# Optimization experiments

Hardware: AMD Instinct MI355X
Metric: run time of the kernel (lower is better)

Reference implementation:

```python
import jax, jax.numpy as jnp
import numpy as np

N = 100000   # total nodes across the batch
D = 3        # ambient dimension of the point cloud
T = 64       # num_thetas (directions)
R = 64       # resolution of the ECT discretization
B = 128      # number of point clouds in the batch
RADIUS = 1.1
SCALE = 8.0


def setup_inputs() -> dict:
    key = jax.random.key(0)
    kx, kv, kb = jax.random.split(key, 3)
    x = jax.random.normal(kx, (N, D), dtype=jnp.float32)
    # directions; the layer stores v movedim'd and moves it back, so math uses [D, T]
    v = jax.random.normal(kv, (D, T), dtype=jnp.float32)
    v = v / jnp.linalg.norm(v, axis=0, keepdims=True)  # unit directions, typical usage
    batch = jnp.sort(jax.random.randint(kb, (N,), 0, B, dtype=jnp.int64))
    return {"x": x, "v": v, "batch": batch}


def reference(x, v, batch):
    # compute_ect_points:
    # nh[n,t] = <x_n, v_t>
    nh = x @ v  # [N, T]
    lin = jnp.linspace(-RADIUS, RADIUS, R, dtype=x.dtype)  # [R]
    # ecc[n,t,r] = sigmoid(scale * (lin[r] - nh[n,t]))  -- large [N,T,R] intermediate
    ecc = jax.nn.sigmoid(SCALE * (lin[None, None, :] - nh[:, :, None]))
    # scatter-sum over the batch index (index_add): -> [B, T, R]
    ect = jax.ops.segment_sum(ecc, batch, num_segments=B)
    # normalized=False -> return ect.squeeze(); no singleton dims here
    return ect
```

## Files before the change

kernel.cpp:

```cpp
#include <hip/hip_runtime.h>
#include <math.h>


#define THREADS 256
#define TPB 4
#define TQ  16
#define PAD 63
#define STEPS 148
#define ROW32 228
#define ROW64 114
#define HO_BASE64 (TPB * ROW64)

constexpr double cexp_taylor(double r) {
    double s = 1.0, term = 1.0;
    for (int i = 1; i < 18; ++i) { term *= r / (double)i; s += term; }
    return s;
}
constexpr double cexp(double x) {
    const double LN2 = 0.69314718055994530942;
    const int n = (int)(x / LN2 + (x >= 0.0 ? 0.5 : -0.5));
    const double r = x - (double)n * LN2;
    double e = cexp_taylor(r);
    if (n >= 0) { for (int i = 0; i < n;  ++i) e *= 2.0; }
    else        { for (int i = 0; i < -n; ++i) e *= 0.5; }
    return e;
}
struct WTab {
    float w[STEPS];
    constexpr WTab() : w() {
        const double d = 2.2 / 63.0;
        for (int j = 0; j < STEPS; ++j) {
            const double z = 8.0 * d * (double)(111 - j);
            w[j] = (float)(1.0 / ((1.0 + cexp(-z)) * 65536.0));
        }
    }
};
constexpr WTab WT;

__device__ __forceinline__ int lb64(const int* __restrict__ A, int n, int val,
                                    int lane) {
    int lo = 0, hi = n;
    while (hi - lo > 64) {
        const long long span = hi - lo;
        const int p = lo + (int)((span * lane) >> 6);
        const unsigned long long m = __ballot(A[p] < val);
        const int c = __popcll(m);
        if (c == 0) { hi = lo; break; }
        const int plast = lo + (int)((span * (c - 1)) >> 6);
        const int pnext = (c < 64) ? (lo + (int)((span * (long long)c) >> 6)) : hi;
        lo = plast + 1; hi = pnext;
    }
    const int span = hi - lo;
    const unsigned long long m = __ballot(lane < span && A[lo + lane] < val);
    return lo + __popcll(m);
}

__global__ __launch_bounds__(THREADS, 8) void ect_fused6_kernel(
    const float* __restrict__ x,
    const float* __restrict__ v,
    const int*   __restrict__ batch,
    float* __restrict__ out,
    int n, float inv_d, float bias)
{
    __shared__ unsigned long long Hu[2 * TPB * ROW64];

    const int tid  = threadIdx.x;
    const int wv   = tid >> 6;
    const int lane = tid & 63;
    const int b    = blockIdx.x >> 4;
    const int tq   = blockIdx.x & (TQ - 1);

    for (int i = tid; i < 2 * TPB * ROW64; i += THREADS) Hu[i] = 0ull;

    const int s0 = lb64(batch, n, b, lane);
    const int s1 = lb64(batch, n, b + 1, lane);

    const int t_l  = lane >> 4;
    const int slot = (lane & 15) + (wv << 4);
    const int tbase = tq * TPB;
    const int t    = tbase + t_l;
    const float va = v[t], vb = v[64 + t], vc = v[128 + t];
    const int rowoff64 = t_l * ROW64;

    __syncthreads();

    for (int base = s0; base < s1; base += 4 * 64) {
        float xs0[4], xs1[4], xs2[4];
        bool  ok[4];
#pragma unroll
        for (int k = 0; k < 4; ++k) {
            const int idx = base + (k << 6) + slot;
            ok[k] = (idx < s1);
            if (ok[k]) {
                const float3 xx = *(const float3*)(x + 3 * (size_t)idx);
                xs0[k] = xx.x; xs1[k] = xx.y; xs2[k] = xx.z;
            }
        }
#pragma unroll
        for (int k = 0; k < 4; ++k) {
            if (!ok[k]) continue;
            const float nh = fmaf(xs0[k], va, fmaf(xs1[k], vb, xs2[k] * vc));
            float bin = fmaf(nh, inv_d, bias);
            bin = fminf(fmaxf(bin, 0.0f), 158.999f);
            const float g0f = floorf(bin);
            const float fr  = bin - g0f;
            const int   a   = PAD + (int)g0f;
            const unsigned q1 = (unsigned)(fr * 65536.0f + 0.5f);
            const unsigned q0 = 65536u - q1;
            const unsigned long long val =
                (unsigned long long)q0 | ((unsigned long long)q1 << 32);
            const int w64 = (a >> 1) + rowoff64 + ((a & 1) ? HO_BASE64 : 0);
            atomicAdd(&Hu[w64], val);
        }
    }

    __syncthreads();

    {
        unsigned* He32 = (unsigned*)Hu;
        unsigned* Ho32 = (unsigned*)(Hu + HO_BASE64);
        if (tid < ROW32) {
#pragma unroll
            for (int tt = 0; tt < TPB; ++tt) {
                const int i = tt * ROW32 + tid;
                unsigned s = He32[i];
                if (tid > 0) s += Ho32[i - 1];
                ((float*)He32)[i] = (float)s;
            }
        }
    }

    __syncthreads();

    const float* H = (const float*)Hu + wv * ROW32 + lane;
    float a0 = 0.f, a1 = 0.f;
#pragma unroll
    for (int j = 0; j < STEPS; j += 2) {
        a0 = fmaf(WT.w[j],     H[j],     a0);
        a1 = fmaf(WT.w[j + 1], H[j + 1], a1);
    }
    out[((size_t)b * 64 + tbase + wv) * 64 + lane] = a0 + a1;
}

extern "C" void kernel_launch(void* const* d_in, const int* in_sizes, int n_in,
                              void* d_out, int out_size, void* d_ws, size_t ws_size,
                              hipStream_t stream) {
    const float* x     = (const float*)d_in[0];
    const float* v     = (const float*)d_in[1];
    const int*   batch = (const int*)d_in[2];
    float*       out   = (float*)d_out;

    const int n = in_sizes[0] / 3;

    const double d = 2.2 / 63.0;
    const float inv_d = (float)(1.0 / d);
    const float bias  = 79.5f;

    hipLaunchKernelGGL(ect_fused6_kernel, dim3(128 * TQ), dim3(THREADS), 0,
                       stream, x, v, batch, out, n, inv_d, bias);
}
```

Measured before the change: 17.52 us.

## Precompute segment bounds in a separate kernel and shorten weighted sum with suffix sums

A new pre-pass kernel writes per-batch segment start offsets into workspace, which replaces the per-block wave-parallel binary search over the batch array. In the main kernel, the first 60 sigmoid weights are treated as saturated to one. Their contribution is computed as a difference of wave-level suffix sums of the histogram, which leaves fewer FMA steps per output. The cost is a second kernel launch and extra shared memory plus shuffle work. Rows are also widened to 256, which changes the LDS footprint and may reduce occupancy. Treating those weights as exactly one introduces a small approximation error.

New measurement: 20.30 us. 1.16x slower.

```diff
diff --git a/kernel.cpp b/kernel.cpp
--- a/kernel.cpp
+++ b/kernel.cpp
@@ -7,9 +7,11 @@
 #define TQ  16
 #define PAD 63
 #define STEPS 148
-#define ROW32 228
-#define ROW64 114
+#define J0 60
+#define ROW32 256
+#define ROW64 128
 #define HO_BASE64 (TPB * ROW64)
+#define BSEG 128
 
 constexpr double cexp_taylor(double r) {
     double s = 1.0, term = 1.0;
@@ -37,32 +39,40 @@
 };
 constexpr WTab WT;
 
-__device__ __forceinline__ int lb64(const int* __restrict__ A, int n, int val,
-                                    int lane) {
-    int lo = 0, hi = n;
-    while (hi - lo > 64) {
-        const long long span = hi - lo;
-        const int p = lo + (int)((span * lane) >> 6);
-        const unsigned long long m = __ballot(A[p] < val);
-        const int c = __popcll(m);
-        if (c == 0) { hi = lo; break; }
-        const int plast = lo + (int)((span * (c - 1)) >> 6);
-        const int pnext = (c < 64) ? (lo + (int)((span * (long long)c) >> 6)) : hi;
-        lo = plast + 1; hi = pnext;
+__device__ __forceinline__ float wave_suffix(float x, int lane) {
+#pragma unroll
+    for (int d = 1; d < 64; d <<= 1) {
+        const float y = __shfl_down(x, d, 64);
+        x += (lane + d < 64) ? y : 0.0f;
     }
-    const int span = hi - lo;
-    const unsigned long long m = __ballot(lane < span && A[lo + lane] < val);
-    return lo + __popcll(m);
+    return x;
 }
 
-__global__ __launch_bounds__(THREADS, 8) void ect_fused6_kernel(
+__global__ void seg_bounds_kernel(const int* __restrict__ batch,
+                                  int* __restrict__ seg, int n) {
+    int i = blockIdx.x * blockDim.x + threadIdx.x;
+    if (i >= n) return;
+    const int a = batch[i];
+    if (i == 0) {
+        for (int bb = 0; bb <= a; ++bb) seg[bb] = 0;
+    } else {
+        const int p = batch[i - 1];
+        for (int bb = p + 1; bb <= a; ++bb) seg[bb] = i;
+    }
+    if (i == n - 1) {
+        for (int bb = a + 1; bb <= BSEG; ++bb) seg[bb] = n;
+    }
+}
+
+__global__ __launch_bounds__(THREADS, 8) void ect_fused8_kernel(
     const float* __restrict__ x,
     const float* __restrict__ v,
-    const int*   __restrict__ batch,
+    const int*   __restrict__ seg,
     float* __restrict__ out,
-    int n, float inv_d, float bias)
+    float inv_d, float bias)
 {
     __shared__ unsigned long long Hu[2 * TPB * ROW64];
+    __shared__ float Slds[TPB][128];
 
     const int tid  = threadIdx.x;
     const int wv   = tid >> 6;
@@ -72,8 +82,7 @@
 
     for (int i = tid; i < 2 * TPB * ROW64; i += THREADS) Hu[i] = 0ull;
 
-    const int s0 = lb64(batch, n, b, lane);
-    const int s1 = lb64(batch, n, b + 1, lane);
+    const int s0 = seg[b], s1 = seg[b + 1];
 
     const int t_l  = lane >> 4;
     const int slot = (lane & 15) + (wv << 4);
@@ -119,23 +128,37 @@
     {
         unsigned* He32 = (unsigned*)Hu;
         unsigned* Ho32 = (unsigned*)(Hu + HO_BASE64);
-        if (tid < ROW32) {
-#pragma unroll
-            for (int tt = 0; tt < TPB; ++tt) {
-                const int i = tt * ROW32 + tid;
-                unsigned s = He32[i];
-                if (tid > 0) s += Ho32[i - 1];
-                ((float*)He32)[i] = (float)s;
-            }
+        for (int i = tid; i < TPB * ROW32; i += THREADS) {
+            const int a = i & (ROW32 - 1);
+            unsigned s = He32[i];
+            if (a > 0) s += Ho32[i - 1];
+            ((float*)He32)[i] = (float)s;
         }
     }
 
     __syncthreads();
 
+    {
+        const float* HF = (const float*)Hu + wv * ROW32;
+        const float c0 = HF[lane],       c1 = HF[64 + lane];
+        const float c2 = HF[128 + lane], c3 = HF[192 + lane];
+        float tot23 = c2 + c3;
+#pragma unroll
+        for (int d = 1; d < 64; d <<= 1) tot23 += __shfl_xor(tot23, d, 64);
+        const float s1v = wave_suffix(c1, lane) + tot23;
+        const float carry = __shfl(s1v, 0, 64);
+        const float s0v = wave_suffix(c0, lane) + carry;
+        Slds[wv][lane]      = s0v;
+        Slds[wv][64 + lane] = s1v;
+    }
+
+    __syncthreads();
+
     const float* H = (const float*)Hu + wv * ROW32 + lane;
-    float a0 = 0.f, a1 = 0.f;
+    float a0 = (Slds[wv][lane] - Slds[wv][lane + J0]) * (1.0f / 65536.0f);
+    float a1 = 0.f;
 #pragma unroll
-    for (int j = 0; j < STEPS; j += 2) {
+    for (int j = J0; j < STEPS; j += 2) {
         a0 = fmaf(WT.w[j],     H[j],     a0);
         a1 = fmaf(WT.w[j + 1], H[j + 1], a1);
     }
@@ -152,10 +175,14 @@
 
     const int n = in_sizes[0] / 3;
 
+    int* seg = (int*)d_ws;
+
     const double d = 2.2 / 63.0;
     const float inv_d = (float)(1.0 / d);
     const float bias  = 79.5f;
 
-    hipLaunchKernelGGL(ect_fused6_kernel, dim3(128 * TQ), dim3(THREADS), 0,
-                       stream, x, v, batch, out, n, inv_d, bias);
+    hipLaunchKernelGGL(seg_bounds_kernel, dim3((n + THREADS - 1) / THREADS),
+                       dim3(THREADS), 0, stream, batch, seg, n);
+    hipLaunchKernelGGL(ect_fused8_kernel, dim3(BSEG * TQ), dim3(THREADS), 0,
+                       stream, x, v, seg, out, inv_d, bias);
 }
```

## Replace saturated sigmoid taps with suffix-sum window and use guessed scalar segment search

Applied to the files above, without the earlier changes.

The per-output convolution over 148 sigmoid weights is shortened to 80 taps. The far bins where the weight is essentially 1 are folded into a single suffix sum computed with wave shuffles, and the histogram rows are padded to 256 so each wave converts its own row. The wave-wide ballot lower-bound search is replaced by a scalar binary search that starts from a window guessed from a uniform batch distribution and falls back to a full search if the guess is wrong. This saves FMA and LDS reads in the epilogue but adds shuffle reductions and treats weights beyond the window as exactly 1, which is a slight approximation.

New measurement: 17.80 us. About the same (+1.6%).

```diff
diff --git a/kernel.cpp b/kernel.cpp
--- a/kernel.cpp
+++ b/kernel.cpp
@@ -6,10 +6,12 @@
 #define TPB 4
 #define TQ  16
 #define PAD 63
-#define STEPS 148
-#define ROW32 228
-#define ROW64 114
+#define J0  64
+#define STEPS 144
+#define ROW32 256
+#define ROW64 128
 #define HO_BASE64 (TPB * ROW64)
+#define BSEG 128
 
 constexpr double cexp_taylor(double r) {
     double s = 1.0, term = 1.0;
@@ -37,25 +39,32 @@
 };
 constexpr WTab WT;
 
-__device__ __forceinline__ int lb64(const int* __restrict__ A, int n, int val,
-                                    int lane) {
-    int lo = 0, hi = n;
-    while (hi - lo > 64) {
-        const long long span = hi - lo;
-        const int p = lo + (int)((span * lane) >> 6);
-        const unsigned long long m = __ballot(A[p] < val);
-        const int c = __popcll(m);
-        if (c == 0) { hi = lo; break; }
-        const int plast = lo + (int)((span * (c - 1)) >> 6);
-        const int pnext = (c < 64) ? (lo + (int)((span * (long long)c) >> 6)) : hi;
-        lo = plast + 1; hi = pnext;
+__device__ __forceinline__ float wave_suffix(float x, int lane) {
+#pragma unroll
+    for (int d = 1; d < 64; d <<= 1) {
+        const float y = __shfl_down(x, d, 64);
+        x += (lane + d < 64) ? y : 0.0f;
     }
-    const int span = hi - lo;
-    const unsigned long long m = __ballot(lane < span && A[lo + lane] < val);
-    return lo + __popcll(m);
+    return x;
 }
 
-__global__ __launch_bounds__(THREADS, 8) void ect_fused6_kernel(
+__device__ __forceinline__ int lower_scalar(const int* __restrict__ A, int n,
+                                            int val) {
+    const long long g = ((long long)val * (long long)n) >> 7;
+    int lo = (int)(g - 1024 > 0 ? g - 1024 : 0);
+    int hi = (int)(g + 1024 < n ? g + 1024 : n);
+    const bool okl = (lo == 0) || (A[__builtin_amdgcn_readfirstlane(lo - 1)] < val);
+    const bool okh = (hi == n) || (A[__builtin_amdgcn_readfirstlane(hi)] >= val);
+    if (!(okl && okh)) { lo = 0; hi = n; }
+    while (hi > lo) {
+        const int mid = (lo + hi) >> 1;
+        const int key = A[__builtin_amdgcn_readfirstlane(mid)];
+        if (key < val) lo = mid + 1; else hi = mid;
+    }
+    return lo;
+}
+
+__global__ __launch_bounds__(THREADS, 8) void ect_fused9_kernel(
     const float* __restrict__ x,
     const float* __restrict__ v,
     const int*   __restrict__ batch,
@@ -72,8 +81,8 @@
 
     for (int i = tid; i < 2 * TPB * ROW64; i += THREADS) Hu[i] = 0ull;
 
-    const int s0 = lb64(batch, n, b, lane);
-    const int s1 = lb64(batch, n, b + 1, lane);
+    const int s0 = lower_scalar(batch, n, b);
+    const int s1 = lower_scalar(batch, n, b + 1);
 
     const int t_l  = lane >> 4;
     const int slot = (lane & 15) + (wv << 4);
@@ -116,26 +125,36 @@
 
     __syncthreads();
 
+    float c[4];
     {
-        unsigned* He32 = (unsigned*)Hu;
-        unsigned* Ho32 = (unsigned*)(Hu + HO_BASE64);
-        if (tid < ROW32) {
+        const unsigned* He32 = (const unsigned*)Hu;
+        const unsigned* Ho32 = (const unsigned*)(Hu + HO_BASE64);
+        float* Hf = (float*)Hu;
+        const int rb = wv * ROW32;
 #pragma unroll
-            for (int tt = 0; tt < TPB; ++tt) {
-                const int i = tt * ROW32 + tid;
-                unsigned s = He32[i];
-                if (tid > 0) s += Ho32[i - 1];
-                ((float*)He32)[i] = (float)s;
-            }
+        for (int q = 0; q < 4; ++q) {
+            const int a = lane + 64 * q;
+            unsigned s = He32[rb + a];
+            if (a > 0) s += Ho32[rb + a - 1];
+            c[q] = (float)s;
+            if (q > 0) Hf[rb + a] = c[q];
         }
     }
+
+    float tot23 = c[2] + c[3];
+#pragma unroll
+    for (int d = 1; d < 64; d <<= 1) tot23 += __shfl_xor(tot23, d, 64);
+    const float s1v   = wave_suffix(c[1], lane) + tot23;
+    const float carry = __shfl(s1v, 0, 64);
+    const float s0v   = wave_suffix(c[0], lane) + carry;
+    const float window = (s0v - s1v) * (1.0f / 65536.0f);
 
     __syncthreads();
 
     const float* H = (const float*)Hu + wv * ROW32 + lane;
-    float a0 = 0.f, a1 = 0.f;
+    float a0 = window, a1 = 0.f;
 #pragma unroll
-    for (int j = 0; j < STEPS; j += 2) {
+    for (int j = J0; j < STEPS; j += 2) {
         a0 = fmaf(WT.w[j],     H[j],     a0);
         a1 = fmaf(WT.w[j + 1], H[j + 1], a1);
     }
@@ -156,6 +175,6 @@
     const float inv_d = (float)(1.0 / d);
     const float bias  = 79.5f;
 
-    hipLaunchKernelGGL(ect_fused6_kernel, dim3(128 * TQ), dim3(THREADS), 0,
+    hipLaunchKernelGGL(ect_fused9_kernel, dim3(BSEG * TQ), dim3(THREADS), 0,
                        stream, x, v, batch, out, n, inv_d, bias);
 }
```
